# Kernel tuning notes

Hardware: AMD Instinct MI355X
Metric: run time of the kernel (lower is better)

Reference implementation:

```python
import jax, jax.numpy as jnp
import numpy as np

B, N, FIN, H, D = 8, 2048, 64, 4, 32
ALPHA = 0.2  # LeakyReLU negative slope


def setup_inputs() -> dict:
    key = jax.random.key(0)
    k1, k2, k3, k4 = jax.random.split(key, 4)
    h = jax.random.normal(k1, (B, N, FIN), dtype=jnp.float32)
    adj = jax.random.randint(k2, (B, N, N), 0, 2).astype(jnp.int32)
    # ensure self-loops so every softmax row has at least one unmasked entry
    idx = jnp.arange(N)
    adj = adj.at[:, idx, idx].set(1)
    W = jax.random.normal(k3, (FIN, H * D), dtype=jnp.float32) * 0.1
    a = jax.random.normal(k4, (H, 2 * D), dtype=jnp.float32) * 0.1
    return {"h": h, "adj": adj, "W": W, "a": a}


def reference(h, adj, W, a):
    # h: (B,N,Fin), adj: (B,N,N) int, W: (Fin,H*D), a: (H,2D)
    Bn, Nn, _ = h.shape
    Hh, twoD = a.shape
    Dd = twoD // 2
    Wh = (h @ W).reshape(Bn, Nn, Hh, Dd).transpose(0, 2, 1, 3)  # (B,H,N,D)
    # e_ij = leakyrelu(Wh_i . a1 + Wh_j . a2) -- avoids O(N^2 * 2D) concat
    src = jnp.einsum('bhnd,hd->bhn', Wh, a[:, :Dd])  # (B,H,N)
    dst = jnp.einsum('bhnd,hd->bhn', Wh, a[:, Dd:])  # (B,H,N)
    e = jax.nn.leaky_relu(src[:, :, :, None] + dst[:, :, None, :], negative_slope=ALPHA)  # (B,H,N,N)
    e = jnp.where(adj[:, None, :, :] == 0, -jnp.inf, e)
    attn = jax.nn.softmax(e, axis=-1)  # (B,H,N,N)
    out = jnp.einsum('bhij,bhjd->bhid', attn, Wh)  # (B,H,N,D)
    return out.transpose(0, 2, 1, 3).reshape(Bn, Nn, Hh * Dd)
```

## Files before the change

kernel.cpp:

```cpp
#include <hip/hip_runtime.h>

typedef short short8 __attribute__((ext_vector_type(8)));
typedef _Float16 half8 __attribute__((ext_vector_type(8)));
typedef _Float16 half2v __attribute__((ext_vector_type(2)));
typedef float floatx4 __attribute__((ext_vector_type(4)));

extern "C" __device__ _Float16 __ocml_exp2_f16(_Float16);

#define B_   8
#define N_   2048
#define FIN_ 64
#define H_   4
#define D_   32
#define HD_  128
#define ALPHA_ 0.2f
#define LOG2E_ 1.4426950408889634f


__global__ __launch_bounds__(256) void gat_prep4(
    const float* __restrict__ h, const float* __restrict__ W, const float* __restrict__ a,
    unsigned short* __restrict__ WhF, float* __restrict__ src, unsigned short* __restrict__ dstb)
{
    __shared__ float Ws[FIN_][HD_];
    __shared__ float hsT[FIN_][36];
    int bx = blockIdx.x;
    int b = bx >> 6;
    int n0 = (bx & 63) * 32;
    int tid = threadIdx.x;

    #pragma unroll
    for (int it = 0; it < 8; ++it) {
        int idx = it * 256 + tid;
        int k = idx >> 5, c4 = (idx & 31) << 2;
        *(float4*)&Ws[k][c4] = *(const float4*)&W[k * HD_ + c4];
    }
    #pragma unroll
    for (int it = 0; it < 8; ++it) {
        int idx = it * 256 + tid;
        int r = idx >> 6, k = idx & 63;
        hsT[k][r] = h[((size_t)b * N_ + n0 + r) * FIN_ + k];
    }
    __syncthreads();

    int c = tid & 127;
    int rq = tid >> 7;
    int hh = c >> 5, d = c & 31;
    float acc[16];
    #pragma unroll
    for (int r = 0; r < 16; ++r) acc[r] = 0.f;
    for (int k = 0; k < FIN_; ++k) {
        float wv = Ws[k][c];
        float4 h0 = *(const float4*)&hsT[k][rq * 16];
        float4 h1 = *(const float4*)&hsT[k][rq * 16 + 4];
        float4 h2 = *(const float4*)&hsT[k][rq * 16 + 8];
        float4 h3 = *(const float4*)&hsT[k][rq * 16 + 12];
        acc[0]  += h0.x * wv; acc[1]  += h0.y * wv; acc[2]  += h0.z * wv; acc[3]  += h0.w * wv;
        acc[4]  += h1.x * wv; acc[5]  += h1.y * wv; acc[6]  += h1.z * wv; acc[7]  += h1.w * wv;
        acc[8]  += h2.x * wv; acc[9]  += h2.y * wv; acc[10] += h2.z * wv; acc[11] += h2.w * wv;
        acc[12] += h3.x * wv; acc[13] += h3.y * wv; acc[14] += h3.z * wv; acc[15] += h3.w * wv;
    }

    {
        int half = d >> 4, n = d & 15;
        int j0 = n0 + rq * 16;
        int it0 = j0 >> 5;
        int g0 = (j0 >> 3) & 3;
        #pragma unroll
        for (int rr = 0; rr < 2; ++rr) {
            __attribute__((aligned(16))) unsigned pk4[4];
            #pragma unroll
            for (int q = 0; q < 4; ++q)
                pk4[q] = __builtin_bit_cast(unsigned,
                    __builtin_amdgcn_cvt_pkrtz(acc[rr * 8 + 2 * q], acc[rr * 8 + 2 * q + 1]));
            size_t fi = ((((size_t)b * H_ + hh) * 64 + it0) * 2 + half) * 64
                        + (size_t)(g0 + rr) * 16 + n;
            *(uint4*)&WhF[fi * 8] = *(uint4*)pk4;
        }
    }

    float a1v = a[hh * 64 + d];
    float a2v = a[hh * 64 + 32 + d];
    #pragma unroll
    for (int r = 0; r < 16; ++r) {
        float s1 = acc[r] * a1v;
        float s2 = acc[r] * a2v;
        #pragma unroll
        for (int off = 16; off >= 1; off >>= 1) {
            s1 += __shfl_xor(s1, off, 32);
            s2 += __shfl_xor(s2, off, 32);
        }
        if (d == 0) {
            int n = n0 + rq * 16 + r;
            src[(b * H_ + hh) * N_ + n] = s1 * LOG2E_;
            _Float16 hv = (_Float16)(s2 * LOG2E_);
            dstb[(b * H_ + hh) * N_ + n] = __builtin_bit_cast(unsigned short, hv);
        }
    }
}

__global__ __launch_bounds__(256, 4) void gat_main14(
    const int* __restrict__ adj, const unsigned short* __restrict__ WhF,
    const float* __restrict__ src, const unsigned short* __restrict__ dstb,
    float* __restrict__ out)
{
    __shared__ unsigned short dsts[H_ * N_];
    __shared__ unsigned adjW[16][72];

    int bx = blockIdx.x;
    int b  = bx >> 7;
    int i0 = (bx & 127) * 16;
    int tid = threadIdx.x;
    int wv = tid >> 6, l = tid & 63;

    #pragma unroll
    for (int it = 0; it < 4; ++it) {
        int idx = it * 256 + tid;
        int hh = idx >> 8, off = (idx & 255) * 8;
        *(uint4*)&dsts[hh * N_ + off] =
            *(const uint4*)&dstb[(size_t)(b * H_ + hh) * N_ + off];
    }

    const int* adjBase = adj + ((size_t)(b * N_ + i0 + wv * 4)) * N_ + l;

    int vals[16];
    #pragma unroll
    for (int rr = 0; rr < 4; ++rr)
        #pragma unroll
        for (int cc = 0; cc < 4; ++cc)
            vals[rr * 4 + cc] = adjBase[rr * N_ + cc * 64];

    int h = wv, g = l >> 4, m = l & 15;
    int g8 = g << 3;
    _Float16 sv = (_Float16)src[(b * H_ + h) * N_ + i0 + m];
    half2v s2; s2[0] = sv; s2[1] = sv;
    const _Float16 alf = (_Float16)0.2f;
    const unsigned short* WhB =
        WhF + ((size_t)(b * H_ + h) * 64) * 1024 + l * 8;
    const unsigned short* dstH = &dsts[h * N_];

    short8 onesS;
    #pragma unroll
    for (int q = 0; q < 8; ++q) onesS[q] = (short)0x3C00;
    half8 ones = __builtin_bit_cast(half8, onesS);

    floatx4 acc0 = {0.f, 0.f, 0.f, 0.f};
    floatx4 acc1 = {0.f, 0.f, 0.f, 0.f};
    floatx4 acc2 = {0.f, 0.f, 0.f, 0.f};

    short8 bf0_a = *(const short8*)&WhB[0];
    short8 bf1_a = *(const short8*)&WhB[512];
    short8 bf0_b = *(const short8*)&WhB[1024];
    short8 bf1_b = *(const short8*)&WhB[1536];
    uint4 dv_a, dv_b;

    for (int q = 0; q < 8; ++q) {
        #pragma unroll
        for (int rr = 0; rr < 4; ++rr)
            #pragma unroll
            for (int cc = 0; cc < 4; ++cc) {
                unsigned long long mk = __ballot(vals[rr * 4 + cc] != 0);
                if (l == 0)
                    *(unsigned long long*)&adjW[wv * 4 + rr][2 * (q * 4 + cc)] = mk;
            }
        __syncthreads();

        uint4 shv0 = *(const uint4*)&adjW[m][q * 8];
        uint4 shv1 = *(const uint4*)&adjW[m][q * 8 + 4];
        if (q == 0) {
            dv_a = *(const uint4*)&dstH[g8];
            dv_b = *(const uint4*)&dstH[32 + g8];
        }

        if (q < 7) {
            #pragma unroll
            for (int rr = 0; rr < 4; ++rr)
                #pragma unroll
                for (int cc = 0; cc < 4; ++cc)
                    vals[rr * 4 + cc] = adjBase[rr * N_ + (q + 1) * 256 + cc * 64];
        }

        #pragma unroll
        for (int jj = 0; jj < 8; ++jj) {
            int it = q * 8 + jj;
            int fn = (it + 2) * 1024;
            short8 bf0_n = *(const short8*)&WhB[fn];
            short8 bf1_n = *(const short8*)&WhB[fn + 512];
            int j2 = ((it + 2) << 5) + g8;
            uint4  dv_n = *(const uint4*)&dstH[(j2 < N_) ? j2 : g8];

            unsigned sh = (jj < 4 ? ((const unsigned*)&shv0)[jj]
                                  : ((const unsigned*)&shv1)[jj - 4]) >> g8;
            const unsigned* du = (const unsigned*)&dv_a;
            __attribute__((aligned(16))) unsigned pk[4];
            #pragma unroll
            for (int c2 = 0; c2 < 4; ++c2) {
                half2v d2 = __builtin_bit_cast(half2v, du[c2]);
                half2v e2 = s2 + d2;
                half2v t2 = e2 * alf;
                e2 = __builtin_elementwise_max(e2, t2);
                half2v x2;
                x2[0] = __ocml_exp2_f16(e2[0]);
                x2[1] = __ocml_exp2_f16(e2[1]);
                unsigned mk = ((((sh >> (2 * c2 + 1)) & 1u) << 16)
                               | ((sh >> (2 * c2)) & 1u)) * 0x3C00u;
                x2 = x2 * __builtin_bit_cast(half2v, mk);
                pk[c2] = __builtin_bit_cast(unsigned, x2);
            }
            half8 af = __builtin_bit_cast(half8, *(uint4*)pk);
            acc0 = __builtin_amdgcn_mfma_f32_16x16x32_f16(
                       af, __builtin_bit_cast(half8, bf0_a), acc0, 0, 0, 0);
            acc1 = __builtin_amdgcn_mfma_f32_16x16x32_f16(
                       af, __builtin_bit_cast(half8, bf1_a), acc1, 0, 0, 0);
            acc2 = __builtin_amdgcn_mfma_f32_16x16x32_f16(af, ones, acc2, 0, 0, 0);
            bf0_a = bf0_b; bf0_b = bf0_n;
            bf1_a = bf1_b; bf1_b = bf1_n;
            dv_a = dv_b;   dv_b = dv_n;
        }
    }

    #pragma unroll
    for (int r = 0; r < 4; ++r) {
        float inv = 1.f / acc2[r];
        size_t o = ((size_t)b * N_ + i0 + g * 4 + r) * HD_ + h * 32 + m;
        out[o]      = acc0[r] * inv;
        out[o + 16] = acc1[r] * inv;
    }
}

extern "C" void kernel_launch(void* const* d_in, const int* in_sizes, int n_in,
                              void* d_out, int out_size, void* d_ws, size_t ws_size,
                              hipStream_t stream) {
    const float* h   = (const float*)d_in[0];
    const int*   adj = (const int*)d_in[1];
    const float* W   = (const float*)d_in[2];
    const float* a   = (const float*)d_in[3];
    float* out = (float*)d_out;

    unsigned short* WhF  = (unsigned short*)d_ws;
    float*          src  = (float*)((char*)d_ws + 4u * 1024 * 1024);
    unsigned short* dstb = (unsigned short*)((char*)d_ws + 4u * 1024 * 1024 + 256u * 1024);

    gat_prep4<<<B_ * (N_ / 32), 256, 0, stream>>>(h, W, a, WhF, src, dstb);
    gat_main14<<<B_ * (N_ / 16), 256, 0, stream>>>(adj, WhF, src, dstb, out);
}
```

Baseline: 218.9 us.

## Stage adjacency as additive fp16 -inf mask in double-buffered LDS

Replaces the ballot-based bitmask packing of adjacency with per-thread int2 loads converted into fp16 additive masks (-inf for absent edges) stored in a double-buffered LDS array laid out for the MFMA fragment. The mask is added before the LeakyReLU and exp2, which drops the bit-extraction and multiply. Adjacency loads are prefetched two chunks ahead. This removes the wave ballots and the lane-0 stores, at the cost of more LDS traffic and more registers for the prefetched values.

```diff
diff --git a/kernel.cpp b/kernel.cpp
--- a/kernel.cpp
+++ b/kernel.cpp
@@ -98,13 +98,27 @@
     }
 }
 
-__global__ __launch_bounds__(256, 4) void gat_main14(
+#define LOADG(Q, V)                                                     \
+    _Pragma("unroll")                                                   \
+    for (int cc = 0; cc < 8; ++cc)                                      \
+        V[cc] = adjR[(Q) * 128 + cc * 16 + ps];
+
+#define STAGE(Q, V)                                                     \
+    _Pragma("unroll")                                                   \
+    for (int cc = 0; cc < 8; ++cc) {                                    \
+        int2 v_ = V[cc];                                                \
+        unsigned w_ = (v_.x == 0 ? 0xFC00u : 0u)                        \
+                    | (v_.y == 0 ? 0xFC000000u : 0u);                   \
+        maskM[(Q) & 1][cc][psg16 + row][ps & 3] = w_;                   \
+    }
+
+__global__ __launch_bounds__(256, 4) void gat_main19(
     const int* __restrict__ adj, const unsigned short* __restrict__ WhF,
     const float* __restrict__ src, const unsigned short* __restrict__ dstb,
     float* __restrict__ out)
 {
     __shared__ unsigned short dsts[H_ * N_];
-    __shared__ unsigned adjW[16][72];
+    __shared__ unsigned maskM[2][8][64][4];
 
     int bx = blockIdx.x;
     int b  = bx >> 7;
@@ -112,6 +126,15 @@
     int tid = threadIdx.x;
     int wv = tid >> 6, l = tid & 63;
 
+    int ps    = l >> 2;
+    int row   = wv * 4 + (l & 3);
+    int psg16 = (ps >> 2) * 16;
+    const int2* adjR = (const int2*)(adj + ((size_t)(b * N_ + i0 + row)) * N_);
+
+    int2 valsA[8], valsB[8];
+    LOADG(0, valsA);
+    LOADG(1, valsB);
+
     #pragma unroll
     for (int it = 0; it < 4; ++it) {
         int idx = it * 256 + tid;
@@ -119,15 +142,6 @@
         *(uint4*)&dsts[hh * N_ + off] =
             *(const uint4*)&dstb[(size_t)(b * H_ + hh) * N_ + off];
     }
-
-    const int* adjBase = adj + ((size_t)(b * N_ + i0 + wv * 4)) * N_ + l;
-
-    int vals[16];
-    #pragma unroll
-    for (int rr = 0; rr < 4; ++rr)
-        #pragma unroll
-        for (int cc = 0; cc < 4; ++cc)
-            vals[rr * 4 + cc] = adjBase[rr * N_ + cc * 64];
 
     int h = wv, g = l >> 4, m = l & 15;
     int g8 = g << 3;
@@ -138,14 +152,14 @@
         WhF + ((size_t)(b * H_ + h) * 64) * 1024 + l * 8;
     const unsigned short* dstH = &dsts[h * N_];
 
-    short8 onesS;
-    #pragma unroll
-    for (int q = 0; q < 8; ++q) onesS[q] = (short)0x3C00;
-    half8 ones = __builtin_bit_cast(half8, onesS);
-
     floatx4 acc0 = {0.f, 0.f, 0.f, 0.f};
     floatx4 acc1 = {0.f, 0.f, 0.f, 0.f};
     floatx4 acc2 = {0.f, 0.f, 0.f, 0.f};
+
+    short8 onesS;
+    #pragma unroll
+    for (int q = 0; q < 8; ++q) onesS[q] = (short)0x3C00;
+    half8 ones = __builtin_bit_cast(half8, onesS);
 
     short8 bf0_a = *(const short8*)&WhB[0];
     short8 bf1_a = *(const short8*)&WhB[512];
@@ -153,32 +167,7 @@
     short8 bf1_b = *(const short8*)&WhB[1536];
     uint4 dv_a, dv_b;
 
-    for (int q = 0; q < 8; ++q) {
-        #pragma unroll
-        for (int rr = 0; rr < 4; ++rr)
-            #pragma unroll
-            for (int cc = 0; cc < 4; ++cc) {
-                unsigned long long mk = __ballot(vals[rr * 4 + cc] != 0);
-                if (l == 0)
-                    *(unsigned long long*)&adjW[wv * 4 + rr][2 * (q * 4 + cc)] = mk;
-            }
-        __syncthreads();
-
-        uint4 shv0 = *(const uint4*)&adjW[m][q * 8];
-        uint4 shv1 = *(const uint4*)&adjW[m][q * 8 + 4];
-        if (q == 0) {
-            dv_a = *(const uint4*)&dstH[g8];
-            dv_b = *(const uint4*)&dstH[32 + g8];
-        }
-
-        if (q < 7) {
-            #pragma unroll
-            for (int rr = 0; rr < 4; ++rr)
-                #pragma unroll
-                for (int cc = 0; cc < 4; ++cc)
-                    vals[rr * 4 + cc] = adjBase[rr * N_ + (q + 1) * 256 + cc * 64];
-        }
-
+    auto compute = [&](int q) {
         #pragma unroll
         for (int jj = 0; jj < 8; ++jj) {
             int it = q * 8 + jj;
@@ -188,22 +177,21 @@
             int j2 = ((it + 2) << 5) + g8;
             uint4  dv_n = *(const uint4*)&dstH[(j2 < N_) ? j2 : g8];
 
-            unsigned sh = (jj < 4 ? ((const unsigned*)&shv0)[jj]
-                                  : ((const unsigned*)&shv1)[jj - 4]) >> g8;
+            uint4 mv = *(const uint4*)&maskM[q & 1][jj][l][0];
             const unsigned* du = (const unsigned*)&dv_a;
+            const unsigned* mu = (const unsigned*)&mv;
             __attribute__((aligned(16))) unsigned pk[4];
             #pragma unroll
             for (int c2 = 0; c2 < 4; ++c2) {
                 half2v d2 = __builtin_bit_cast(half2v, du[c2]);
+                half2v m2 = __builtin_bit_cast(half2v, mu[c2]);
                 half2v e2 = s2 + d2;
+                e2 = e2 + m2;
                 half2v t2 = e2 * alf;
                 e2 = __builtin_elementwise_max(e2, t2);
                 half2v x2;
                 x2[0] = __ocml_exp2_f16(e2[0]);
                 x2[1] = __ocml_exp2_f16(e2[1]);
-                unsigned mk = ((((sh >> (2 * c2 + 1)) & 1u) << 16)
-                               | ((sh >> (2 * c2)) & 1u)) * 0x3C00u;
-                x2 = x2 * __builtin_bit_cast(half2v, mk);
                 pk[c2] = __builtin_bit_cast(unsigned, x2);
             }
             half8 af = __builtin_bit_cast(half8, *(uint4*)pk);
@@ -216,6 +204,24 @@
             bf1_a = bf1_b; bf1_b = bf1_n;
             dv_a = dv_b;   dv_b = dv_n;
         }
+    };
+
+    for (int qq = 0; qq < 4; ++qq) {
+        int q0 = 2 * qq, q1 = 2 * qq + 1;
+
+        STAGE(q0, valsA);
+        __syncthreads();
+        if (qq == 0) {
+            dv_a = *(const uint4*)&dstH[g8];
+            dv_b = *(const uint4*)&dstH[32 + g8];
+        }
+        if (qq < 3) LOADG(q0 + 2, valsA);
+        compute(q0);
+
+        STAGE(q1, valsB);
+        __syncthreads();
+        if (qq < 3) LOADG(q1 + 2, valsB);
+        compute(q1);
     }
 
     #pragma unroll
@@ -241,5 +247,5 @@
     unsigned short* dstb = (unsigned short*)((char*)d_ws + 4u * 1024 * 1024 + 256u * 1024);
 
     gat_prep4<<<B_ * (N_ / 32), 256, 0, stream>>>(h, W, a, WhF, src, dstb);
-    gat_main14<<<B_ * (N_ / 16), 256, 0, stream>>>(adj, WhF, src, dstb, out);
+    gat_main19<<<B_ * (N_ / 16), 256, 0, stream>>>(adj, WhF, src, dstb, out);
 }
```

New measurement: 250.0 us. +14.2%, slower.
